# Kernel tuning notes

Measured on AMD Instinct MI355X. Metric: run time of the kernel, lower is better.

Reference implementation:

```python
import jax, jax.numpy as jnp
import numpy as np

N_TOKENS = 8192
MODEL_DIM = 4096
NUM_EXPERTS = 64


def setup_inputs() -> dict:
    key = jax.random.key(0)
    k1, k2 = jax.random.split(key)
    x = jax.random.normal(k1, (N_TOKENS, MODEL_DIM), dtype=jnp.float32)
    wg = jax.random.normal(k2, (NUM_EXPERTS, MODEL_DIM), dtype=jnp.float32) * (MODEL_DIM ** -0.5)
    return {"x": x, "wg": wg, "top_k": 2}


def reference(x, wg, top_k):
    # logits: [N, E]
    logits = jnp.einsum("nd,ed->ne", x, wg)
    N, E = logits.shape
    _, idx = jax.lax.top_k(logits, top_k)            # idx: [N, K]
    gates = jax.nn.softmax(logits, axis=1)           # [N, E]
    masks = jax.nn.one_hot(idx.T, E, dtype=jnp.float32)  # [K, N, E]
    # gate value for each chosen expert: (gates * mask).sum(-1) == gather
    gates_k = jnp.take_along_axis(gates, idx, axis=1).T  # [K, N]
    # load-balance loss (fp32 branch of original)
    me = jnp.sum(gates, axis=0)                      # [E]
    ce = jnp.sum(masks[0], axis=0)                   # [E]
    l_loss = jnp.sum(me * ce) * (E / (N * N))
    # cumsum-based location assignment: position of each token in its expert's buffer
    csum = jnp.cumsum(masks, axis=1) - 1.0           # [K, N, E], fast_cumsum_sub_one
    col = jnp.sum(masks, axis=1)                     # [K, E] per-k expert counts
    acc = jnp.cumsum(col, axis=0) - col              # exclusive prefix over k (acc_base)
    locations = jnp.sum((csum + acc[:, None, :]) * masks, axis=2).astype(jnp.int32)  # [K, N]
    if top_k > 1:
        denom = jnp.clip(jnp.sum(gates_k, axis=0), jnp.finfo(gates_k.dtype).eps, None)
        gates_k = gates_k / denom
    return l_loss, gates_k, idx.T.astype(jnp.int32), locations
```

## Files before the change

### kernel.cpp

```cpp
#include <hip/hip_runtime.h>
#include <cmath>
#include <cstdint>
#include <cstddef>

#define NT 8192
#define MD 4096
#define NE 64
#define NCHUNK 128

static constexpr int OFF_GATES = 1;
static constexpr int OFF_IDX   = 1 + 2 * NT;
static constexpr int OFF_LOC   = 1 + 4 * NT;

typedef __attribute__((ext_vector_type(8))) short short8_t;
typedef __attribute__((ext_vector_type(4))) float f32x4;

#define BM    64
#define KSTEP 32
#define ROWP  40

__device__ __forceinline__ void split3(float v, short& h, short& m, short& s) {
  unsigned bx = __float_as_uint(v);
  h = (short)(bx >> 16);
  float r1 = v - __uint_as_float(bx & 0xFFFF0000u);
  unsigned b1 = __float_as_uint(r1);
  m = (short)(b1 >> 16);
  float r2 = r1 - __uint_as_float(b1 & 0xFFFF0000u);
  s = (short)(__float_as_uint(r2) >> 16);
}

__global__ __launch_bounds__(256, 2)
void k1_gemm(const float* __restrict__ x, const float* __restrict__ wg,
             float* __restrict__ part, int kchunk) {
  __shared__ short Ah[2][BM * ROWP], Am[2][BM * ROWP], As[2][BM * ROWP];
  __shared__ short Bh[2][NE * ROWP], Bm[2][NE * ROWP], Bs[2][NE * ROWP];
  const int tid  = threadIdx.x;
  const int lane = tid & 63;
  const int w    = tid >> 6;
  const int mt   = blockIdx.x;
  const int kc   = blockIdx.y * kchunk;
  const int NS   = kchunk / KSTEP;

  const int srow = tid >> 2;
  const int soct = tid & 3;
  const float* xsrc = x  + (size_t)(mt * BM + srow) * MD + kc + soct * 8;
  const float* wsrc = wg + (size_t)srow * MD + kc + soct * 8;

  f32x4 acc[4];
#pragma unroll
  for (int n = 0; n < 4; ++n) acc[n] = (f32x4){0.f, 0.f, 0.f, 0.f};

  float4 rx0, rx1, rw0, rw1;
  auto load_regs = [&](int s) {
    const float4* p = (const float4*)(xsrc + (size_t)s * KSTEP);
    rx0 = p[0]; rx1 = p[1];
    const float4* q = (const float4*)(wsrc + (size_t)s * KSTEP);
    rw0 = q[0]; rw1 = q[1];
  };

  const int soff = srow * ROWP + soct * 8;
  auto cvt_write = [&](int buf) {
    float vx[8] = {rx0.x, rx0.y, rx0.z, rx0.w, rx1.x, rx1.y, rx1.z, rx1.w};
    float vw[8] = {rw0.x, rw0.y, rw0.z, rw0.w, rw1.x, rw1.y, rw1.z, rw1.w};
    short8_t h, m, s;
#pragma unroll
    for (int i = 0; i < 8; ++i) { short a, b, c; split3(vx[i], a, b, c); h[i] = a; m[i] = b; s[i] = c; }
    *(short8_t*)&Ah[buf][soff] = h;
    *(short8_t*)&Am[buf][soff] = m;
    *(short8_t*)&As[buf][soff] = s;
#pragma unroll
    for (int i = 0; i < 8; ++i) { short a, b, c; split3(vw[i], a, b, c); h[i] = a; m[i] = b; s[i] = c; }
    *(short8_t*)&Bh[buf][soff] = h;
    *(short8_t*)&Bm[buf][soff] = m;
    *(short8_t*)&Bs[buf][soff] = s;
  };

  const int aoff = (w * 16 + (lane & 15)) * ROWP + (lane >> 4) * 8;
  const int boff0 = (lane & 15) * ROWP + (lane >> 4) * 8;

  auto compute = [&](int buf) {
    short8_t a_h = *(const short8_t*)&Ah[buf][aoff];
    short8_t a_m = *(const short8_t*)&Am[buf][aoff];
    short8_t a_s = *(const short8_t*)&As[buf][aoff];
#pragma unroll
    for (int n = 0; n < 4; ++n) {
      const int bo = boff0 + n * 16 * ROWP;
      short8_t b_h = *(const short8_t*)&Bh[buf][bo];
      short8_t b_m = *(const short8_t*)&Bm[buf][bo];
      short8_t b_s = *(const short8_t*)&Bs[buf][bo];
      acc[n] = __builtin_amdgcn_mfma_f32_16x16x32_bf16(a_h, b_h, acc[n], 0, 0, 0);
      acc[n] = __builtin_amdgcn_mfma_f32_16x16x32_bf16(a_h, b_m, acc[n], 0, 0, 0);
      acc[n] = __builtin_amdgcn_mfma_f32_16x16x32_bf16(a_m, b_h, acc[n], 0, 0, 0);
      acc[n] = __builtin_amdgcn_mfma_f32_16x16x32_bf16(a_h, b_s, acc[n], 0, 0, 0);
      acc[n] = __builtin_amdgcn_mfma_f32_16x16x32_bf16(a_s, b_h, acc[n], 0, 0, 0);
      acc[n] = __builtin_amdgcn_mfma_f32_16x16x32_bf16(a_m, b_m, acc[n], 0, 0, 0);
    }
  };

  load_regs(0);
  cvt_write(0);
  __syncthreads();

  int buf = 0;
  for (int s = 0; s < NS; ++s) {
    if (s + 1 < NS) load_regs(s + 1);
    compute(buf);
    if (s + 1 < NS) cvt_write(buf ^ 1);
    __syncthreads();
    buf ^= 1;
  }

  const int c   = blockIdx.y;
  const int col = lane & 15;
  const int rq  = lane >> 4;
#pragma unroll
  for (int n = 0; n < 4; ++n)
#pragma unroll
    for (int r = 0; r < 4; ++r) {
      const int tok = mt * BM + w * 16 + rq * 4 + r;
      part[((size_t)c * NT + tok) * NE + n * 16 + col] = acc[n][r];
    }
}

__global__ void k2a_reduce(float* __restrict__ part, int ks) {
  const size_t i = (size_t)blockIdx.x * blockDim.x + threadIdx.x;
  float4* p = (float4*)part;
  float4 v = p[i];
  for (int c = 1; c < ks; ++c) {
    float4 u = p[(size_t)c * (NT * NE / 4) + i];
    v.x += u.x; v.y += u.y; v.z += u.z; v.w += u.w;
  }
  p[i] = v;
}

__global__ void k2b_topk(const float* __restrict__ part, float* __restrict__ out,
                         float* __restrict__ me_partial,
                         int* __restrict__ cnt0, int* __restrict__ cnt1,
                         int* __restrict__ rank0, int* __restrict__ rank1) {
  const int lane  = threadIdx.x;
  const int chunk = blockIdx.x;
  const int token = chunk * 64 + lane;

  float l[NE];
  const float4* p4 = (const float4*)(part + (size_t)token * NE);
#pragma unroll
  for (int q = 0; q < 16; ++q) {
    float4 v = p4[q];
    l[4*q+0] = v.x; l[4*q+1] = v.y; l[4*q+2] = v.z; l[4*q+3] = v.w;
  }

  float m1 = -INFINITY; int i1 = 0;
#pragma unroll
  for (int e = 0; e < NE; ++e) if (l[e] > m1) { m1 = l[e]; i1 = e; }
  float m2 = -INFINITY; int i2 = 0;
#pragma unroll
  for (int e = 0; e < NE; ++e) if (e != i1 && l[e] > m2) { m2 = l[e]; i2 = e; }

  float s = 0.f;
#pragma unroll
  for (int e = 0; e < NE; ++e) { l[e] = __expf(l[e] - m1); s += l[e]; }
  const float inv_s = 1.f / s;

  const float g2 = __expf(m2 - m1);
  const float dn = 1.f + g2;
  out[OFF_GATES + token]      = 1.f / dn;
  out[OFF_GATES + NT + token] = g2 / dn;
  out[OFF_IDX + token]        = (float)i1;
  out[OFF_IDX + NT + token]   = (float)i2;

  const unsigned long long below = (1ULL << lane) - 1ULL;
  for (int e = 0; e < NE; ++e) {
    unsigned long long ma = __ballot(i1 == e);
    unsigned long long mb = __ballot(i2 == e);
    if (i1 == e) rank0[token] = __popcll(ma & below);
    if (i2 == e) rank1[token] = __popcll(mb & below);
    if (lane == e) {
      cnt0[chunk * NE + e] = __popcll(ma);
      cnt1[chunk * NE + e] = __popcll(mb);
    }
  }

  __shared__ float lds[64 * 65];
#pragma unroll
  for (int e = 0; e < NE; ++e) lds[lane * 65 + e] = l[e] * inv_s;
  __syncthreads();
  float col = 0.f;
#pragma unroll
  for (int t = 0; t < 64; ++t) col += lds[t * 65 + lane];
  me_partial[chunk * NE + lane] = col;
}

__global__ void k3b_scan(const int* __restrict__ cnt0, const int* __restrict__ cnt1,
                         int* __restrict__ base0, int* __restrict__ base1,
                         const float* __restrict__ me_partial,
                         float* __restrict__ out) {
  const int e = threadIdx.x;
  int run = 0;
  for (int c = 0; c < NCHUNK; ++c) { base0[c * NE + e] = run; run += cnt0[c * NE + e]; }
  const int ce = run;
  for (int c = 0; c < NCHUNK; ++c) { base1[c * NE + e] = run; run += cnt1[c * NE + e]; }
  float me = 0.f;
  for (int c = 0; c < NCHUNK; ++c) me += me_partial[c * NE + e];
  float v = me * (float)ce;
#pragma unroll
  for (int off = 1; off < 64; off <<= 1) v += __shfl_xor(v, off, 64);
  if (e == 0) out[0] = v * ((float)NE / ((float)NT * (float)NT));
}

__global__ void k3c_loc(float* __restrict__ out,
                        const int* __restrict__ base0, const int* __restrict__ base1,
                        const int* __restrict__ rank0, const int* __restrict__ rank1) {
  const int lane  = threadIdx.x;
  const int chunk = blockIdx.x;
  const int token = chunk * 64 + lane;
  const int i1 = (int)out[OFF_IDX + token];
  const int i2 = (int)out[OFF_IDX + NT + token];
  out[OFF_LOC + token]      = (float)(base0[chunk * NE + i1] + rank0[token]);
  out[OFF_LOC + NT + token] = (float)(base1[chunk * NE + i2] + rank1[token]);
}

extern "C" void kernel_launch(void* const* d_in, const int* in_sizes, int n_in,
                              void* d_out, int out_size, void* d_ws, size_t ws_size,
                              hipStream_t stream) {
  const float* x  = (const float*)d_in[0];
  const float* wg = (const float*)d_in[1];
  float* out = (float*)d_out;

  int ks = 4;
  while (ks > 1 &&
         ((size_t)ks * NT * NE + 7 * (size_t)NCHUNK * NE) * sizeof(float) > ws_size)
    ks >>= 1;
  const int kchunk = MD / ks;

  float* part       = (float*)d_ws;
  float* me_partial = part + (size_t)ks * NT * NE;
  int*   cnt0  = (int*)(me_partial + NCHUNK * NE);
  int*   cnt1  = cnt0  + NCHUNK * NE;
  int*   base0 = cnt1  + NCHUNK * NE;
  int*   base1 = base0 + NCHUNK * NE;
  int*   rank0 = base1 + NCHUNK * NE;
  int*   rank1 = rank0 + NT;

  hipLaunchKernelGGL(k1_gemm, dim3(NT / BM, ks), dim3(256), 0, stream,
                     x, wg, part, kchunk);
  if (ks > 1)
    hipLaunchKernelGGL(k2a_reduce, dim3(NT * NE / 4 / 256), dim3(256), 0, stream, part, ks);
  hipLaunchKernelGGL(k2b_topk, dim3(NCHUNK), dim3(64), 0, stream,
                     part, out, me_partial, cnt0, cnt1, rank0, rank1);
  hipLaunchKernelGGL(k3b_scan, dim3(1), dim3(64), 0, stream,
                     cnt0, cnt1, base0, base1, me_partial, out);
  hipLaunchKernelGGL(k3c_loc, dim3(NCHUNK), dim3(64), 0, stream,
                     out, base0, base1, rank0, rank1);
}
```

Baseline: 66.20 us.

## Pre-split gate weights, drop LDS staging in GEMM, fuse reduce into top-k

Adds a pre-pass that splits wg into three bf16 planes once, so the GEMM no longer splits the weights inside every block. The GEMM now reads A directly from global memory into registers and reads B planes from global, with no shared memory or barriers; occupancy hint raised and split-K doubled to 8. The separate partial-sum reduce kernel is removed and its summation folded into the top-k kernel, and the count and me buffers are transposed so the scan reads contiguously. The risk is uncoalesced direct global loads and more partial-sum traffic in exchange for fewer launches and no LDS synchronisation.

New measurement: 153.5 us. 132% more time.

```diff
diff --git a/kernel.cpp b/kernel.cpp
--- a/kernel.cpp
+++ b/kernel.cpp
@@ -14,10 +14,6 @@
 
 typedef __attribute__((ext_vector_type(8))) short short8_t;
 typedef __attribute__((ext_vector_type(4))) float f32x4;
-
-#define BM    64
-#define KSTEP 32
-#define ROWP  40
 
 __device__ __forceinline__ void split3(float v, short& h, short& m, short& s) {
   unsigned bx = __float_as_uint(v);
@@ -29,65 +25,55 @@
   s = (short)(__float_as_uint(r2) >> 16);
 }
 
-__global__ __launch_bounds__(256, 2)
-void k1_gemm(const float* __restrict__ x, const float* __restrict__ wg,
+__global__ __launch_bounds__(256)
+void k0_split(const float* __restrict__ wg, short* __restrict__ bh,
+              short* __restrict__ bm, short* __restrict__ bs) {
+  const int i = (blockIdx.x * 256 + threadIdx.x) * 4;
+  float4 v = *(const float4*)(wg + i);
+  short h0, m0, s0, h1, m1, s1, h2, m2, s2, h3, m3, s3;
+  split3(v.x, h0, m0, s0); split3(v.y, h1, m1, s1);
+  split3(v.z, h2, m2, s2); split3(v.w, h3, m3, s3);
+  *(short4*)(bh + i) = make_short4(h0, h1, h2, h3);
+  *(short4*)(bm + i) = make_short4(m0, m1, m2, m3);
+  *(short4*)(bs + i) = make_short4(s0, s1, s2, s3);
+}
+
+__global__ __launch_bounds__(256, 4)
+void k1_gemm(const float* __restrict__ x, const short* __restrict__ bh,
+             const short* __restrict__ bm, const short* __restrict__ bs,
              float* __restrict__ part, int kchunk) {
-  __shared__ short Ah[2][BM * ROWP], Am[2][BM * ROWP], As[2][BM * ROWP];
-  __shared__ short Bh[2][NE * ROWP], Bm[2][NE * ROWP], Bs[2][NE * ROWP];
-  const int tid  = threadIdx.x;
-  const int lane = tid & 63;
-  const int w    = tid >> 6;
+  const int lane = threadIdx.x & 63;
+  const int w    = threadIdx.x >> 6;
   const int mt   = blockIdx.x;
   const int kc   = blockIdx.y * kchunk;
-  const int NS   = kchunk / KSTEP;
-
-  const int srow = tid >> 2;
-  const int soct = tid & 3;
-  const float* xsrc = x  + (size_t)(mt * BM + srow) * MD + kc + soct * 8;
-  const float* wsrc = wg + (size_t)srow * MD + kc + soct * 8;
+  const int row  = lane & 15;
+  const int koct = lane >> 4;
+
+  const int tok = mt * 64 + w * 16 + row;
+  const float* ap = x + (size_t)tok * MD + kc + koct * 8;
+  const size_t boff = (size_t)row * MD + kc + koct * 8;
 
   f32x4 acc[4];
 #pragma unroll
   for (int n = 0; n < 4; ++n) acc[n] = (f32x4){0.f, 0.f, 0.f, 0.f};
 
-  float4 rx0, rx1, rw0, rw1;
-  auto load_regs = [&](int s) {
-    const float4* p = (const float4*)(xsrc + (size_t)s * KSTEP);
-    rx0 = p[0]; rx1 = p[1];
-    const float4* q = (const float4*)(wsrc + (size_t)s * KSTEP);
-    rw0 = q[0]; rw1 = q[1];
-  };
-
-  const int soff = srow * ROWP + soct * 8;
-  auto cvt_write = [&](int buf) {
-    float vx[8] = {rx0.x, rx0.y, rx0.z, rx0.w, rx1.x, rx1.y, rx1.z, rx1.w};
-    float vw[8] = {rw0.x, rw0.y, rw0.z, rw0.w, rw1.x, rw1.y, rw1.z, rw1.w};
-    short8_t h, m, s;
-#pragma unroll
-    for (int i = 0; i < 8; ++i) { short a, b, c; split3(vx[i], a, b, c); h[i] = a; m[i] = b; s[i] = c; }
-    *(short8_t*)&Ah[buf][soff] = h;
-    *(short8_t*)&Am[buf][soff] = m;
-    *(short8_t*)&As[buf][soff] = s;
-#pragma unroll
-    for (int i = 0; i < 8; ++i) { short a, b, c; split3(vw[i], a, b, c); h[i] = a; m[i] = b; s[i] = c; }
-    *(short8_t*)&Bh[buf][soff] = h;
-    *(short8_t*)&Bm[buf][soff] = m;
-    *(short8_t*)&Bs[buf][soff] = s;
-  };
-
-  const int aoff = (w * 16 + (lane & 15)) * ROWP + (lane >> 4) * 8;
-  const int boff0 = (lane & 15) * ROWP + (lane >> 4) * 8;
-
-  auto compute = [&](int buf) {
-    short8_t a_h = *(const short8_t*)&Ah[buf][aoff];
-    short8_t a_m = *(const short8_t*)&Am[buf][aoff];
-    short8_t a_s = *(const short8_t*)&As[buf][aoff];
+  const int NS = kchunk / 32;
+  for (int s = 0; s < NS; ++s) {
+    float4 a0 = *(const float4*)(ap + s * 32);
+    float4 a1 = *(const float4*)(ap + s * 32 + 4);
+    float av[8] = {a0.x, a0.y, a0.z, a0.w, a1.x, a1.y, a1.z, a1.w};
+    short8_t a_h, a_m, a_s;
+#pragma unroll
+    for (int i = 0; i < 8; ++i) {
+      short h, m, q; split3(av[i], h, m, q);
+      a_h[i] = h; a_m[i] = m; a_s[i] = q;
+    }
 #pragma unroll
     for (int n = 0; n < 4; ++n) {
-      const int bo = boff0 + n * 16 * ROWP;
-      short8_t b_h = *(const short8_t*)&Bh[buf][bo];
-      short8_t b_m = *(const short8_t*)&Bm[buf][bo];
-      short8_t b_s = *(const short8_t*)&Bs[buf][bo];
+      const size_t bo = boff + (size_t)n * 16 * MD + s * 32;
+      short8_t b_h = *(const short8_t*)(bh + bo);
+      short8_t b_m = *(const short8_t*)(bm + bo);
+      short8_t b_s = *(const short8_t*)(bs + bo);
       acc[n] = __builtin_amdgcn_mfma_f32_16x16x32_bf16(a_h, b_h, acc[n], 0, 0, 0);
       acc[n] = __builtin_amdgcn_mfma_f32_16x16x32_bf16(a_h, b_m, acc[n], 0, 0, 0);
       acc[n] = __builtin_amdgcn_mfma_f32_16x16x32_bf16(a_m, b_h, acc[n], 0, 0, 0);
@@ -95,19 +81,6 @@
       acc[n] = __builtin_amdgcn_mfma_f32_16x16x32_bf16(a_s, b_h, acc[n], 0, 0, 0);
       acc[n] = __builtin_amdgcn_mfma_f32_16x16x32_bf16(a_m, b_m, acc[n], 0, 0, 0);
     }
-  };
-
-  load_regs(0);
-  cvt_write(0);
-  __syncthreads();
-
-  int buf = 0;
-  for (int s = 0; s < NS; ++s) {
-    if (s + 1 < NS) load_regs(s + 1);
-    compute(buf);
-    if (s + 1 < NS) cvt_write(buf ^ 1);
-    __syncthreads();
-    buf ^= 1;
   }
 
   const int c   = blockIdx.y;
@@ -117,36 +90,29 @@
   for (int n = 0; n < 4; ++n)
 #pragma unroll
     for (int r = 0; r < 4; ++r) {
-      const int tok = mt * BM + w * 16 + rq * 4 + r;
-      part[((size_t)c * NT + tok) * NE + n * 16 + col] = acc[n][r];
-    }
-}
-
-__global__ void k2a_reduce(float* __restrict__ part, int ks) {
-  const size_t i = (size_t)blockIdx.x * blockDim.x + threadIdx.x;
-  float4* p = (float4*)part;
-  float4 v = p[i];
-  for (int c = 1; c < ks; ++c) {
-    float4 u = p[(size_t)c * (NT * NE / 4) + i];
-    v.x += u.x; v.y += u.y; v.z += u.z; v.w += u.w;
-  }
-  p[i] = v;
+      const int dt = mt * 64 + w * 16 + rq * 4 + r;
+      part[((size_t)c * NT + dt) * NE + n * 16 + col] = acc[n][r];
+    }
 }
 
 __global__ void k2b_topk(const float* __restrict__ part, float* __restrict__ out,
-                         float* __restrict__ me_partial,
-                         int* __restrict__ cnt0, int* __restrict__ cnt1,
-                         int* __restrict__ rank0, int* __restrict__ rank1) {
+                         float* __restrict__ meT,
+                         int* __restrict__ cntT0, int* __restrict__ cntT1,
+                         int* __restrict__ rank0, int* __restrict__ rank1, int ks) {
   const int lane  = threadIdx.x;
   const int chunk = blockIdx.x;
   const int token = chunk * 64 + lane;
 
   float l[NE];
-  const float4* p4 = (const float4*)(part + (size_t)token * NE);
-#pragma unroll
-  for (int q = 0; q < 16; ++q) {
-    float4 v = p4[q];
-    l[4*q+0] = v.x; l[4*q+1] = v.y; l[4*q+2] = v.z; l[4*q+3] = v.w;
+#pragma unroll
+  for (int e = 0; e < NE; ++e) l[e] = 0.f;
+  for (int c = 0; c < ks; ++c) {
+    const float4* p4 = (const float4*)(part + ((size_t)c * NT + token) * NE);
+#pragma unroll
+    for (int q = 0; q < 16; ++q) {
+      float4 v = p4[q];
+      l[4*q+0] += v.x; l[4*q+1] += v.y; l[4*q+2] += v.z; l[4*q+3] += v.w;
+    }
   }
 
   float m1 = -INFINITY; int i1 = 0;
@@ -175,8 +141,8 @@
     if (i1 == e) rank0[token] = __popcll(ma & below);
     if (i2 == e) rank1[token] = __popcll(mb & below);
     if (lane == e) {
-      cnt0[chunk * NE + e] = __popcll(ma);
-      cnt1[chunk * NE + e] = __popcll(mb);
+      cntT0[lane * NCHUNK + chunk] = __popcll(ma);
+      cntT1[lane * NCHUNK + chunk] = __popcll(mb);
     }
   }
 
@@ -187,20 +153,27 @@
   float col = 0.f;
 #pragma unroll
   for (int t = 0; t < 64; ++t) col += lds[t * 65 + lane];
-  me_partial[chunk * NE + lane] = col;
-}
-
-__global__ void k3b_scan(const int* __restrict__ cnt0, const int* __restrict__ cnt1,
-                         int* __restrict__ base0, int* __restrict__ base1,
-                         const float* __restrict__ me_partial,
-                         float* __restrict__ out) {
+  meT[lane * NCHUNK + chunk] = col;
+}
+
+__global__ void k3b_scan(const int* __restrict__ cntT0, const int* __restrict__ cntT1,
+                         int* __restrict__ baseT0, int* __restrict__ baseT1,
+                         const float* __restrict__ meT, float* __restrict__ out) {
   const int e = threadIdx.x;
+  const int* c0 = cntT0 + e * NCHUNK;
+  const int* c1 = cntT1 + e * NCHUNK;
+  int* b0 = baseT0 + e * NCHUNK;
+  int* b1 = baseT1 + e * NCHUNK;
   int run = 0;
-  for (int c = 0; c < NCHUNK; ++c) { base0[c * NE + e] = run; run += cnt0[c * NE + e]; }
+#pragma unroll 4
+  for (int c = 0; c < NCHUNK; ++c) { b0[c] = run; run += c0[c]; }
   const int ce = run;
-  for (int c = 0; c < NCHUNK; ++c) { base1[c * NE + e] = run; run += cnt1[c * NE + e]; }
+#pragma unroll 4
+  for (int c = 0; c < NCHUNK; ++c) { b1[c] = run; run += c1[c]; }
   float me = 0.f;
-  for (int c = 0; c < NCHUNK; ++c) me += me_partial[c * NE + e];
+  const float* mp = meT + e * NCHUNK;
+#pragma unroll 4
+  for (int c = 0; c < NCHUNK; ++c) me += mp[c];
   float v = me * (float)ce;
 #pragma unroll
   for (int off = 1; off < 64; off <<= 1) v += __shfl_xor(v, off, 64);
@@ -208,15 +181,15 @@
 }
 
 __global__ void k3c_loc(float* __restrict__ out,
-                        const int* __restrict__ base0, const int* __restrict__ base1,
+                        const int* __restrict__ baseT0, const int* __restrict__ baseT1,
                         const int* __restrict__ rank0, const int* __restrict__ rank1) {
   const int lane  = threadIdx.x;
   const int chunk = blockIdx.x;
   const int token = chunk * 64 + lane;
   const int i1 = (int)out[OFF_IDX + token];
   const int i2 = (int)out[OFF_IDX + NT + token];
-  out[OFF_LOC + token]      = (float)(base0[chunk * NE + i1] + rank0[token]);
-  out[OFF_LOC + NT + token] = (float)(base1[chunk * NE + i2] + rank1[token]);
+  out[OFF_LOC + token]      = (float)(baseT0[i1 * NCHUNK + chunk] + rank0[token]);
+  out[OFF_LOC + NT + token] = (float)(baseT1[i2 * NCHUNK + chunk] + rank1[token]);
 }
 
 extern "C" void kernel_launch(void* const* d_in, const int* in_sizes, int n_in,
@@ -226,29 +199,35 @@
   const float* wg = (const float*)d_in[1];
   float* out = (float*)d_out;
 
-  int ks = 4;
+  const size_t bsplit_elems = (size_t)NE * MD;
+  const size_t fixed_bytes  = 3 * bsplit_elems * sizeof(short)
+                            + (5 * (size_t)NE * NCHUNK + 2 * NT) * 4;
+  int ks = 8;
   while (ks > 1 &&
-         ((size_t)ks * NT * NE + 7 * (size_t)NCHUNK * NE) * sizeof(float) > ws_size)
+         fixed_bytes + (size_t)ks * NT * NE * sizeof(float) > ws_size)
     ks >>= 1;
   const int kchunk = MD / ks;
 
-  float* part       = (float*)d_ws;
-  float* me_partial = part + (size_t)ks * NT * NE;
-  int*   cnt0  = (int*)(me_partial + NCHUNK * NE);
-  int*   cnt1  = cnt0  + NCHUNK * NE;
-  int*   base0 = cnt1  + NCHUNK * NE;
-  int*   base1 = base0 + NCHUNK * NE;
-  int*   rank0 = base1 + NCHUNK * NE;
-  int*   rank1 = rank0 + NT;
-
-  hipLaunchKernelGGL(k1_gemm, dim3(NT / BM, ks), dim3(256), 0, stream,
-                     x, wg, part, kchunk);
-  if (ks > 1)
-    hipLaunchKernelGGL(k2a_reduce, dim3(NT * NE / 4 / 256), dim3(256), 0, stream, part, ks);
+  short* bh   = (short*)d_ws;
+  short* bm   = bh + bsplit_elems;
+  short* bs   = bm + bsplit_elems;
+  float* part = (float*)(bs + bsplit_elems);
+  float* meT  = part + (size_t)ks * NT * NE;
+  int* cntT0  = (int*)(meT + NE * NCHUNK);
+  int* cntT1  = cntT0 + NE * NCHUNK;
+  int* baseT0 = cntT1 + NE * NCHUNK;
+  int* baseT1 = baseT0 + NE * NCHUNK;
+  int* rank0  = baseT1 + NE * NCHUNK;
+  int* rank1  = rank0 + NT;
+
+  hipLaunchKernelGGL(k0_split, dim3(NE * MD / 1024), dim3(256), 0, stream,
+                     wg, bh, bm, bs);
+  hipLaunchKernelGGL(k1_gemm, dim3(NT / 64, ks), dim3(256), 0, stream,
+                     x, bh, bm, bs, part, kchunk);
   hipLaunchKernelGGL(k2b_topk, dim3(NCHUNK), dim3(64), 0, stream,
-                     part, out, me_partial, cnt0, cnt1, rank0, rank1);
+                     part, out, meT, cntT0, cntT1, rank0, rank1, ks);
   hipLaunchKernelGGL(k3b_scan, dim3(1), dim3(64), 0, stream,
-                     cnt0, cnt1, base0, base1, me_partial, out);
+                     cntT0, cntT1, baseT0, baseT1, meT, out);
   hipLaunchKernelGGL(k3c_loc, dim3(NCHUNK), dim3(64), 0, stream,
-                     out, base0, base1, rank0, rank1);
-}
+                     out, baseT0, baseT1, rank0, rank1);
+}
```
